# Kernel optimization log

Hardware: AMD Instinct MI355X
Metric: run time of the kernel (lower is better)

## Reference

```python
import jax, jax.numpy as jnp
import numpy as np
from jax import lax

# Conv4d decomposed (as in the torch implementation) into a sum of Conv3d's
# over the first spatial kernel axis. Each 3D conv is vectorized by folding
# the strided first-dim slices into the batch dimension.

def conv4d(x, w, b, stride=(2, 2, 2, 2), padding=(1, 1, 1, 1)):
    # x: [B, Ci, D1, D2, D3, D4]; w: [Co, Ci, K1, K2, K3, K4]; b: [Co]
    B, Ci, D1, D2, D3, D4 = x.shape
    Co, _, K1, K2, K3, K4 = w.shape
    s1, p1 = stride[0], padding[0]
    T = (D1 + 2 * p1 - K1) // s1 + 1  # output size along first spatial dim
    xp = jnp.pad(x, ((0, 0), (0, 0), (p1, p1), (0, 0), (0, 0), (0, 0)))
    pad3 = [(padding[j], padding[j]) for j in (1, 2, 3)]
    out = None
    for i in range(K1):  # small fixed loop over kernel taps along dim0
        xi = xp[:, :, i:i + s1 * (T - 1) + 1:s1]           # [B, Ci, T, D2, D3, D4]
        xi = jnp.moveaxis(xi, 2, 1).reshape(B * T, Ci, D2, D3, D4)
        yi = lax.conv_general_dilated(
            xi, w[:, :, i], window_strides=stride[1:], padding=pad3,
            dimension_numbers=('NCDHW', 'OIDHW', 'NCDHW'))
        out = yi if out is None else out + yi
    O2, O3, O4 = out.shape[2], out.shape[3], out.shape[4]
    out = out.reshape(B, T, Co, O2, O3, O4)
    out = jnp.moveaxis(out, 1, 2)                          # [B, Co, T, O2, O3, O4]
    return out + b[None, :, None, None, None, None]


def setup_inputs() -> dict:
    key = jax.random.key(0)
    k0, k1, k2, k3, k4 = jax.random.split(key, 5)
    C, R = 16, 4  # in_channel, mlp_ratio
    H = C * R     # 64
    x = jax.random.normal(k0, (1, C, 32, 32, 32, 32), dtype=jnp.float32)
    w1 = jax.random.normal(k1, (H, C, 3, 3, 3, 3), dtype=jnp.float32) * 0.02
    b1 = jax.random.normal(k2, (H,), dtype=jnp.float32) * 0.02
    w2 = jax.random.normal(k3, (C, H, 3, 3, 3, 3), dtype=jnp.float32) * 0.02
    b2 = jax.random.normal(k4, (C,), dtype=jnp.float32) * 0.02
    return {'x': x, 'w1': w1, 'b1': b1, 'w2': w2, 'b2': b2}


def reference(x, w1, b1, w2, b2):
    h = conv4d(x, w1, b1)                      # [1, 64, 16, 16, 16, 16]
    h = jax.nn.gelu(h, approximate=False)      # exact erf GELU (torch default)
    return conv4d(h, w2, b2)                   # [1, 16, 8, 8, 8, 8]
```

## Files before the change

kernel.cpp:

```cpp
#include <hip/hip_runtime.h>
#include <hip/hip_bf16.h>
#include <math.h>


typedef __attribute__((ext_vector_type(8))) short short8;
typedef __attribute__((ext_vector_type(4))) float f32x4;
typedef __attribute__((ext_vector_type(4))) unsigned int uint4v;

__device__ __forceinline__ unsigned short f2bf(float v) {
    __hip_bfloat16 b = __float2bfloat16(v);
    return *(unsigned short*)&b;
}

__global__ void setup_kernel(const float* __restrict__ w1, const float* __restrict__ w2,
                             const float* __restrict__ b2,
                             unsigned short* __restrict__ w1p, unsigned short* __restrict__ w2p,
                             uint4v* __restrict__ hz, float* __restrict__ out) {
    int b = blockIdx.x, tid = threadIdx.x;
    if (b < 544) {
        int i = b * 256 + tid;
        int kp = i % 136, co = (i / 136) & 63, ci = i / 8704;
        float v = 0.f;
        if (kp < 108 && (kp & 3) < 3) v = w1[(co * 16 + ci) * 81 + (kp >> 2) * 3 + (kp & 3)];
        w1p[i] = f2bf(v);
    } else if (b < 1088) {
        int i = (b - 544) * 256 + tid;
        int kp = i % 136, co = (i / 136) & 15, ci = i / 2176;
        float v = 0.f;
        if (kp < 108 && (kp & 3) < 3) v = w2[(co * 64 + ci) * 81 + (kp >> 2) * 3 + (kp & 3)];
        w2p[i] = f2bf(v);
    } else if (b < 1344) {
        int i = (b - 1088) * 256 + tid;
        out[i] = b2[i >> 12];
    } else {
        int i = (b - 1344) * 256 + tid;
        hz[i] = (uint4v){0, 0, 0, 0};
        int j = i + 704512;
        if (j < 839808) hz[j] = (uint4v){0, 0, 0, 0};
    }
}

__global__ __launch_bounds__(256) void conv1_mfma(
        const float* __restrict__ x, const unsigned short* __restrict__ w1p,
        const float* __restrict__ b1, unsigned short* __restrict__ hpad) {
    __shared__ unsigned short sX[40000];

    const int tid = threadIdx.x;
    const int braw = blockIdx.x;
    const int bid = ((braw & 7) << 7) | (braw >> 3);
    const int t4 = bid & 1, t3 = (bid >> 1) & 7, t2 = (bid >> 4) & 7, t1 = bid >> 7;
    const int bo1 = 2 * t1, bo2 = 2 * t2, bo3 = 2 * t3, bo4 = 8 * t4;
    const int g1b = 2 * bo1 - 1, g2b = 2 * bo2 - 1, g3b = 2 * bo3 - 1, g4b = 2 * bo4 - 1;

    int offs[5], swb[5];
    unsigned mka = 0, mkb = 0;
#pragma unroll
    for (int r = 0; r < 5; ++r) {
        int u = tid + 256 * r;
        bool uok = u < 1125;
        int uu = uok ? u : 0;
        int p = uu % 9, q = uu / 9;
        int i3 = q % 5; q /= 5;
        int i2 = q % 5; int i1 = q / 5;
        int g1 = g1b + i1, g2 = g2b + i2, g3 = g3b + i3;
        bool ok123 = uok & ((unsigned)g1 < 32u) & ((unsigned)g2 < 32u) & ((unsigned)g3 < 32u);
        int g4a = g4b + 2 * p;
        offs[r] = ((g1 * 32 + g2) * 32 + g3) * 32 + g4a;
        if (ok123 && (unsigned)g4a < 32u) mka |= 1u << r;
        if (ok123 && (unsigned)(g4a + 1) < 32u) mkb |= 1u << r;
        swb[r] = 2 * (((i1 * 5 + i2) * 5 + i3) * 20 + 2 * p);
    }

    auto gatherX = [&](int ci, float (&a)[5], float (&b)[5]) {
        const float* xc = x + (size_t)ci * 1048576;
#pragma unroll
        for (int r = 0; r < 5; ++r) {
            float va = 0.f, vb = 0.f;
            if ((mka >> r) & 1) va = xc[offs[r]];
            if ((mkb >> r) & 1) vb = xc[offs[r] + 1];
            a[r] = va; b[r] = vb;
        }
    };
    auto writeSlab = [&](int ci, const float (&a)[5], const float (&b)[5]) {
        char* slab = (char*)sX + ci * 5000;
#pragma unroll
        for (int r = 0; r < 4; ++r)
            *(unsigned*)(slab + swb[r]) = (unsigned)f2bf(a[r]) | ((unsigned)f2bf(b[r]) << 16);
        if (tid < 101)
            *(unsigned*)(slab + swb[4]) = (unsigned)f2bf(a[4]) | ((unsigned)f2bf(b[4]) << 16);
    };

    const int lane = tid & 63, wv = tid >> 6;
    const int n16 = lane & 15, hi = lane >> 4;
    const int ct0 = 2 * (wv & 1);
    const int st0 = 2 * (wv >> 1);

    int fpb[2];
#pragma unroll
    for (int tt = 0; tt < 2; ++tt) {
        int sp = (st0 + tt) * 16 + n16;
        int o4l = sp & 7, o3l = (sp >> 3) & 1, o2l = (sp >> 4) & 1, o1l = sp >> 5;
        fpb[tt] = 2 * (1000 * o1l + 200 * o2l + 40 * o3l + 2 * o4l);
    }
    int kof[4][2];
#pragma unroll
    for (int ks = 0; ks < 4; ++ks)
#pragma unroll
    for (int j = 0; j < 2; ++j) {
        int g = 8 * ks + 2 * hi + j;
        if (g > 26) g = 26;
        int k1 = g / 9, k2 = (g / 3) % 3, k3 = g % 3;
        kof[ks][j] = 2 * (500 * k1 + 100 * k2 + 20 * k3);
    }

    auto loadA = [&](int ci, short8 (&Ac)[8]) {
        const unsigned short* aw0 = w1p + (size_t)(ci * 64 + 16 * ct0 + n16) * 136 + hi * 8;
#pragma unroll
        for (int k = 0; k < 4; ++k) Ac[k] = *(const short8*)(aw0 + 32 * k);
        const unsigned short* aw1 = aw0 + 16 * 136;
#pragma unroll
        for (int k = 0; k < 4; ++k) Ac[4 + k] = *(const short8*)(aw1 + 32 * k);
    };
    auto readFR = [&](int ci, short8 (&fr)[2][4]) {
        const char* sx = (const char*)sX + ci * 5000;
#pragma unroll
        for (int tt = 0; tt < 2; ++tt) {
            const char* base = sx + fpb[tt];
#pragma unroll
            for (int ks = 0; ks < 4; ++ks) {
                unsigned r0 = *(const unsigned*)(base + kof[ks][0]);
                unsigned r1 = *(const unsigned*)(base + kof[ks][0] + 4);
                unsigned r2 = *(const unsigned*)(base + kof[ks][1]);
                unsigned r3 = *(const unsigned*)(base + kof[ks][1] + 4);
                uint4v t = (uint4v){r0, r1, r2, r3};
                fr[tt][ks] = *(short8*)&t;
            }
        }
    };

    f32x4 acc[2][2];
#pragma unroll
    for (int c = 0; c < 2; ++c)
#pragma unroll
    for (int t = 0; t < 2; ++t) acc[c][t] = (f32x4){0.f, 0.f, 0.f, 0.f};

    auto mfma16 = [&](const short8 (&Ac)[8], const short8 (&fr)[2][4]) {
        __builtin_amdgcn_s_setprio(1);
#pragma unroll
        for (int tt = 0; tt < 2; ++tt)
#pragma unroll
        for (int ks = 0; ks < 4; ++ks) {
            acc[0][tt] = __builtin_amdgcn_mfma_f32_16x16x32_bf16(Ac[ks],     fr[tt][ks], acc[0][tt], 0, 0, 0);
            acc[1][tt] = __builtin_amdgcn_mfma_f32_16x16x32_bf16(Ac[4 + ks], fr[tt][ks], acc[1][tt], 0, 0, 0);
        }
        __builtin_amdgcn_s_setprio(0);
    };

    short8 A0[8], A1[8], F0[2][4], F1[2][4];
    loadA(0, A0);
    loadA(1, A1);

    {
        float a0[5], b0[5], a1[5], b1v[5];
        gatherX(0, a0, b0);
        gatherX(1, a1, b1v);
        for (int cc = 0; cc < 16; cc += 2) {
            writeSlab(cc, a0, b0);
            if (cc + 2 < 16) gatherX(cc + 2, a0, b0);
            writeSlab(cc + 1, a1, b1v);
            if (cc + 3 < 16) gatherX(cc + 3, a1, b1v);
        }
    }
    __syncthreads();

    readFR(0, F0);
    for (int cc = 0; cc < 16; cc += 2) {
        readFR(cc + 1, F1);
        mfma16(A0, F0);
        if (cc < 14) { loadA(cc + 2, A0); readFR(cc + 2, F0); }
        mfma16(A1, F1);
        if (cc < 14) loadA(cc + 3, A1);
    }

#pragma unroll
    for (int c = 0; c < 2; ++c) {
#pragma unroll
        for (int tt = 0; tt < 2; ++tt) {
            int spl = 16 * (st0 + tt) + n16;
            int e4 = spl & 7, e3 = (spl >> 3) & 1, e2 = (spl >> 4) & 1, e1 = spl >> 5;
            size_t base = (size_t)(bo1 + e1 + 1) * 5832 + (bo2 + e2 + 1) * 324 +
                          (bo3 + e3 + 1) * 18 + (bo4 + e4 + 1);
#pragma unroll
            for (int r = 0; r < 4; ++r) {
                int co = 16 * (ct0 + c) + 4 * hi + r;
                float v = acc[c][tt][r] + b1[co];
                v = 0.5f * v * (1.f + erff(v * 0.70710678118654752f));
                hpad[(size_t)co * 104976 + base] = f2bf(v);
            }
        }
    }
}

__global__ __launch_bounds__(256) void conv2_mfma(
        const unsigned short* __restrict__ hpad, const unsigned short* __restrict__ w2p,
        float* __restrict__ out) {
    __shared__ unsigned short sX[20000];

    const int tid = threadIdx.x;
    const int braw = blockIdx.x;
    const int bid = ((braw & 7) << 6) | (braw >> 3);
    const int s = bid & 63, cig = bid >> 6;
    const int t3 = s & 3, t2 = (s >> 2) & 3, t1 = s >> 4;
    const int bo1 = 2 * t1, bo2 = 2 * t2, bo3 = 2 * t3;

    int offs[5], swb[5];
#pragma unroll
    for (int r = 0; r < 5; ++r) {
        int u = tid + 256 * r;
        if (u >= 1125) u = 0;
        int p = u % 9, q = u / 9;
        int i3 = q % 5; q /= 5;
        int i2 = q % 5; int i1 = q / 5;
        offs[r] = (2 * bo1 + i1) * 5832 + (2 * bo2 + i2) * 324 + (2 * bo3 + i3) * 18 + 2 * p;
        swb[r] = 2 * (((i1 * 5 + i2) * 5 + i3) * 20 + 2 * p);
    }

    {
        unsigned fa[5], na[5];
        const unsigned short* h0 = hpad + (size_t)(cig * 8) * 104976;
#pragma unroll
        for (int r = 0; r < 5; ++r) fa[r] = *(const unsigned*)(h0 + offs[r]);
        for (int s8 = 0; s8 < 8; ++s8) {
            if (s8 < 7) {
                const unsigned short* hc = hpad + (size_t)(cig * 8 + s8 + 1) * 104976;
#pragma unroll
                for (int r = 0; r < 5; ++r) na[r] = *(const unsigned*)(hc + offs[r]);
            }
            char* slab = (char*)sX + s8 * 5000;
#pragma unroll
            for (int r = 0; r < 4; ++r) *(unsigned*)(slab + swb[r]) = fa[r];
            if (tid < 101) *(unsigned*)(slab + swb[4]) = fa[4];
            if (s8 < 7) {
#pragma unroll
                for (int r = 0; r < 5; ++r) fa[r] = na[r];
            }
        }
    }
    __syncthreads();

    const int lane = tid & 63, wv = tid >> 6;
    const int n16 = lane & 15, hi = lane >> 4;

    int fpb;
    {
        int sp = wv * 16 + n16;
        int o4l = sp & 7, o3l = (sp >> 3) & 1, o2l = (sp >> 4) & 1, o1l = sp >> 5;
        fpb = 2 * (1000 * o1l + 200 * o2l + 40 * o3l + 2 * o4l);
    }
    int kof[4][2];
#pragma unroll
    for (int ks = 0; ks < 4; ++ks)
#pragma unroll
    for (int j = 0; j < 2; ++j) {
        int g = 8 * ks + 2 * hi + j;
        if (g > 26) g = 26;
        int k1 = g / 9, k2 = (g / 3) % 3, k3 = g % 3;
        kof[ks][j] = 2 * (500 * k1 + 100 * k2 + 20 * k3);
    }

    auto loadA = [&](int s8, short8 (&Ac)[4]) {
        const unsigned short* aw = w2p + (size_t)((cig * 8 + s8) * 16 + n16) * 136 + hi * 8;
#pragma unroll
        for (int k = 0; k < 4; ++k) Ac[k] = *(const short8*)(aw + 32 * k);
    };
    auto readFR = [&](int s8, short8 (&fr)[4]) {
        const char* base = (const char*)sX + s8 * 5000 + fpb;
#pragma unroll
        for (int ks = 0; ks < 4; ++ks) {
            unsigned r0 = *(const unsigned*)(base + kof[ks][0]);
            unsigned r1 = *(const unsigned*)(base + kof[ks][0] + 4);
            unsigned r2 = *(const unsigned*)(base + kof[ks][1]);
            unsigned r3 = *(const unsigned*)(base + kof[ks][1] + 4);
            uint4v tmp = (uint4v){r0, r1, r2, r3};
            fr[ks] = *(short8*)&tmp;
        }
    };

    f32x4 acc = (f32x4){0.f, 0.f, 0.f, 0.f};
    short8 A0[4], A1[4], F0[4], F1[4];
    loadA(0, A0);
    loadA(1, A1);
    readFR(0, F0);

    auto mfma4 = [&](const short8 (&Ac)[4], const short8 (&fr)[4]) {
        __builtin_amdgcn_s_setprio(1);
#pragma unroll
        for (int ks = 0; ks < 4; ++ks)
            acc = __builtin_amdgcn_mfma_f32_16x16x32_bf16(Ac[ks], fr[ks], acc, 0, 0, 0);
        __builtin_amdgcn_s_setprio(0);
    };

    for (int cc = 0; cc < 8; cc += 2) {
        readFR(cc + 1, F1);
        mfma4(A0, F0);
        if (cc < 6) { loadA(cc + 2, A0); readFR(cc + 2, F0); }
        mfma4(A1, F1);
        if (cc < 6) loadA(cc + 3, A1);
    }

    {
        int spl = 16 * wv + n16;
        int e4 = spl & 7, e3 = (spl >> 3) & 1, e2 = (spl >> 4) & 1, e1 = spl >> 5;
        int o1 = bo1 + e1, o2 = bo2 + e2, o3 = bo3 + e3, o4 = e4;
#pragma unroll
        for (int r = 0; r < 4; ++r) {
            int co = 4 * hi + r;
            atomicAdd(&out[(size_t)co * 4096 + o1 * 512 + o2 * 64 + o3 * 8 + o4], acc[r]);
        }
    }
}

extern "C" void kernel_launch(void* const* d_in, const int* in_sizes, int n_in,
                              void* d_out, int out_size, void* d_ws, size_t ws_size,
                              hipStream_t stream) {
    const float* x  = (const float*)d_in[0];
    const float* w1 = (const float*)d_in[1];
    const float* b1 = (const float*)d_in[2];
    const float* w2 = (const float*)d_in[3];
    const float* b2 = (const float*)d_in[4];
    float* out = (float*)d_out;

    unsigned short* hpad = (unsigned short*)d_ws;
    unsigned short* w1p  = hpad + 6718464;
    unsigned short* w2p  = w1p + 139264;

    setup_kernel<<<4096, 256, 0, stream>>>(w1, w2, b2, w1p, w2p, (uint4v*)hpad, out);
    conv1_mfma<<<1024, 256, 0, stream>>>(x, w1p, b1, hpad);
    conv2_mfma<<<512, 256, 0, stream>>>(hpad, w2p, out);
}
```

Baseline: 79.54 us.

## Split conv1 input channels across blocks with fp32 atomic partials and separate GELU pass

conv1 is split into two channel groups of 8 input channels each, doubling the grid to 2048 blocks and halving shared memory per block so occupancy rises. Partial sums are accumulated with fp32 atomics into a new fp32 intermediate buffer that setup must zero. A new gelu_pack kernel adds the bias, applies GELU and writes the padded bf16 tensor. The cost is an extra 16MB fp32 buffer that gets zeroed, written atomically and re-read, plus one more kernel launch.

Result: slower. 150.6 us (+89.4%).

```diff
diff --git a/kernel.cpp b/kernel.cpp
--- a/kernel.cpp
+++ b/kernel.cpp
@@ -15,7 +15,8 @@
 __global__ void setup_kernel(const float* __restrict__ w1, const float* __restrict__ w2,
                              const float* __restrict__ b2,
                              unsigned short* __restrict__ w1p, unsigned short* __restrict__ w2p,
-                             uint4v* __restrict__ hz, float* __restrict__ out) {
+                             uint4v* __restrict__ hz, uint4v* __restrict__ h32z,
+                             float* __restrict__ out) {
     int b = blockIdx.x, tid = threadIdx.x;
     if (b < 544) {
         int i = b * 256 + tid;
@@ -32,23 +33,39 @@
     } else if (b < 1344) {
         int i = (b - 1088) * 256 + tid;
         out[i] = b2[i >> 12];
-    } else {
+    } else if (b < 4096) {
         int i = (b - 1344) * 256 + tid;
         hz[i] = (uint4v){0, 0, 0, 0};
         int j = i + 704512;
         if (j < 839808) hz[j] = (uint4v){0, 0, 0, 0};
-    }
-}
-
-__global__ __launch_bounds__(256) void conv1_mfma(
+    } else {
+        int i = (b - 4096) * 256 + tid;
+        h32z[i] = (uint4v){0, 0, 0, 0};
+    }
+}
+
+__global__ void gelu_pack(const float* __restrict__ h32, const float* __restrict__ b1,
+                          unsigned short* __restrict__ hpad) {
+    int i = blockIdx.x * 256 + threadIdx.x;
+    int co = i >> 16;
+    int sp = i & 65535;
+    int o1 = sp >> 12, o2 = (sp >> 8) & 15, o3 = (sp >> 4) & 15, o4 = sp & 15;
+    float v = h32[i] + b1[co];
+    v = 0.5f * v * (1.f + erff(v * 0.70710678118654752f));
+    hpad[(size_t)co * 104976 + (o1 + 1) * 5832 + (o2 + 1) * 324 + (o3 + 1) * 18 + (o4 + 1)] = f2bf(v);
+}
+
+__global__ __launch_bounds__(256) void conv1_part(
         const float* __restrict__ x, const unsigned short* __restrict__ w1p,
-        const float* __restrict__ b1, unsigned short* __restrict__ hpad) {
-    __shared__ unsigned short sX[40000];
+        float* __restrict__ h32) {
+    __shared__ unsigned short sX[20000];
 
     const int tid = threadIdx.x;
     const int braw = blockIdx.x;
-    const int bid = ((braw & 7) << 7) | (braw >> 3);
-    const int t4 = bid & 1, t3 = (bid >> 1) & 7, t2 = (bid >> 4) & 7, t1 = bid >> 7;
+    const int bid = ((braw & 7) << 8) | (braw >> 3);
+    const int tile = bid & 1023, cig = bid >> 10;
+    const int cb = cig * 8;
+    const int t4 = tile & 1, t3 = (tile >> 1) & 7, t2 = (tile >> 4) & 7, t1 = tile >> 7;
     const int bo1 = 2 * t1, bo2 = 2 * t2, bo3 = 2 * t3, bo4 = 8 * t4;
     const int g1b = 2 * bo1 - 1, g2b = 2 * bo2 - 1, g3b = 2 * bo3 - 1, g4b = 2 * bo4 - 1;
 
@@ -81,8 +98,8 @@
             a[r] = va; b[r] = vb;
         }
     };
-    auto writeSlab = [&](int ci, const float (&a)[5], const float (&b)[5]) {
-        char* slab = (char*)sX + ci * 5000;
+    auto writeSlab = [&](int s, const float (&a)[5], const float (&b)[5]) {
+        char* slab = (char*)sX + s * 5000;
 #pragma unroll
         for (int r = 0; r < 4; ++r)
             *(unsigned*)(slab + swb[r]) = (unsigned)f2bf(a[r]) | ((unsigned)f2bf(b[r]) << 16);
@@ -121,8 +138,8 @@
 #pragma unroll
         for (int k = 0; k < 4; ++k) Ac[4 + k] = *(const short8*)(aw1 + 32 * k);
     };
-    auto readFR = [&](int ci, short8 (&fr)[2][4]) {
-        const char* sx = (const char*)sX + ci * 5000;
+    auto readFR = [&](int s, short8 (&fr)[2][4]) {
+        const char* sx = (const char*)sX + s * 5000;
 #pragma unroll
         for (int tt = 0; tt < 2; ++tt) {
             const char* base = sx + fpb[tt];
@@ -157,29 +174,29 @@
     };
 
     short8 A0[8], A1[8], F0[2][4], F1[2][4];
-    loadA(0, A0);
-    loadA(1, A1);
+    loadA(cb, A0);
+    loadA(cb + 1, A1);
 
     {
         float a0[5], b0[5], a1[5], b1v[5];
-        gatherX(0, a0, b0);
-        gatherX(1, a1, b1v);
-        for (int cc = 0; cc < 16; cc += 2) {
+        gatherX(cb, a0, b0);
+        gatherX(cb + 1, a1, b1v);
+        for (int cc = 0; cc < 8; cc += 2) {
             writeSlab(cc, a0, b0);
-            if (cc + 2 < 16) gatherX(cc + 2, a0, b0);
+            if (cc + 2 < 8) gatherX(cb + cc + 2, a0, b0);
             writeSlab(cc + 1, a1, b1v);
-            if (cc + 3 < 16) gatherX(cc + 3, a1, b1v);
+            if (cc + 3 < 8) gatherX(cb + cc + 3, a1, b1v);
         }
     }
     __syncthreads();
 
     readFR(0, F0);
-    for (int cc = 0; cc < 16; cc += 2) {
+    for (int cc = 0; cc < 8; cc += 2) {
         readFR(cc + 1, F1);
         mfma16(A0, F0);
-        if (cc < 14) { loadA(cc + 2, A0); readFR(cc + 2, F0); }
+        if (cc < 6) { loadA(cb + cc + 2, A0); readFR(cc + 2, F0); }
         mfma16(A1, F1);
-        if (cc < 14) loadA(cc + 3, A1);
+        if (cc < 6) loadA(cb + cc + 3, A1);
     }
 
 #pragma unroll
@@ -188,14 +205,11 @@
         for (int tt = 0; tt < 2; ++tt) {
             int spl = 16 * (st0 + tt) + n16;
             int e4 = spl & 7, e3 = (spl >> 3) & 1, e2 = (spl >> 4) & 1, e1 = spl >> 5;
-            size_t base = (size_t)(bo1 + e1 + 1) * 5832 + (bo2 + e2 + 1) * 324 +
-                          (bo3 + e3 + 1) * 18 + (bo4 + e4 + 1);
+            int sp_lin = (bo1 + e1) * 4096 + (bo2 + e2) * 256 + (bo3 + e3) * 16 + (bo4 + e4);
 #pragma unroll
             for (int r = 0; r < 4; ++r) {
                 int co = 16 * (ct0 + c) + 4 * hi + r;
-                float v = acc[c][tt][r] + b1[co];
-                v = 0.5f * v * (1.f + erff(v * 0.70710678118654752f));
-                hpad[(size_t)co * 104976 + base] = f2bf(v);
+                atomicAdd(&h32[(size_t)co * 65536 + sp_lin], acc[c][tt][r]);
             }
         }
     }
@@ -333,8 +347,11 @@
     unsigned short* hpad = (unsigned short*)d_ws;
     unsigned short* w1p  = hpad + 6718464;
     unsigned short* w2p  = w1p + 139264;
-
-    setup_kernel<<<4096, 256, 0, stream>>>(w1, w2, b2, w1p, w2p, (uint4v*)hpad, out);
-    conv1_mfma<<<1024, 256, 0, stream>>>(x, w1p, b1, hpad);
+    float*          h32  = (float*)(w2p + 139264);
+
+    setup_kernel<<<8192, 256, 0, stream>>>(w1, w2, b2, w1p, w2p,
+                                           (uint4v*)hpad, (uint4v*)h32, out);
+    conv1_part<<<2048, 256, 0, stream>>>(x, w1p, h32);
+    gelu_pack<<<16384, 256, 0, stream>>>(h32, b1, hpad);
     conv2_mfma<<<512, 256, 0, stream>>>(hpad, w2p, out);
 }
```
